# Performance work log

Hardware: AMD Instinct MI355X
Metric: run time of the kernel (lower is better)

The kernel has to match this reference:

```python
import jax, jax.numpy as jnp
import numpy as np

NC = 6          # num_classes
KP = 8          # num_prototype_per_class
NPROTO = NC * KP
PH, PW = 4, 4   # patch grid (num_h, num_w)
MOM = 0.999
EPS = 1e-6


def _layernorm(x, g, b):
    mu = jnp.mean(x, axis=-1, keepdims=True)
    var = jnp.var(x, axis=-1, keepdims=True)
    return (x - mu) / jnp.sqrt(var + EPS) * g + b


def _patch_split(x, nh, nw):
    # (B,C,H,W) -> (B*nh*nw, C, H//nh, W//nw)
    B, C, H, W = x.shape
    ph, pw = H // nh, W // nw
    x = x.reshape(B, C, nh, ph, nw, pw).transpose(0, 2, 4, 1, 3, 5)
    return x.reshape(B * nh * nw, C, ph, pw)


def setup_inputs() -> dict:
    key = jax.random.key(0)
    k1, k2, k3 = jax.random.split(key, 3)
    B, C, Hh, Wh = 8, 128, 128, 128
    Horg, Worg = 512, 512
    return {
        "feats": jax.random.normal(k1, (B, C, Hh, Wh), dtype=jnp.float32),
        "gt": jax.random.randint(k2, (B, Horg, Worg), 0, 7, dtype=jnp.int64),
        "prototype": jax.random.normal(k3, (NPROTO, C), dtype=jnp.float32),
        "ln1_gamma": jnp.ones((C,), jnp.float32),
        "ln1_beta": jnp.zeros((C,), jnp.float32),
        "ln2_gamma": jnp.ones((NPROTO,), jnp.float32),
        "ln2_beta": jnp.zeros((NPROTO,), jnp.float32),
    }


def reference(feats, gt, prototype, ln1_gamma, ln1_beta, ln2_gamma, ln2_beta):
    B, C, Hh, Wh = feats.shape
    Horg, Worg = gt.shape[1], gt.shape[2]

    # --- nearest-neighbor downsample of gt to head resolution (torch 'nearest')
    ih = (jnp.arange(Hh) * Horg) // Hh
    iw = (jnp.arange(Wh) * Worg) // Wh
    label = gt[:, ih[:, None], iw[None, :]]                      # (B,Hh,Wh)
    mask = (label.astype(jnp.int32) != NC).astype(label.dtype)
    one_hot = jax.nn.one_hot(label * mask, NC, dtype=jnp.float32)  # (B,Hh,Wh,NC)
    # torch code does a raw .view(B,-1,Hh,Wh) on the contiguous one-hot; replicate
    pred0 = one_hot.reshape(B, NC, Hh, Wh)

    # --- patch split + spatial gather (softmax-weighted class centers per patch)
    pf = _patch_split(feats, PH, PW)                             # (B*16, C, ph, pw)
    pp = _patch_split(pred0, PH, PW)                             # (B*16, NC, ph, pw)
    bp = pf.shape[0]
    probs = jax.nn.softmax(pp.reshape(bp, NC, -1), axis=2)       # (B*16, NC, HWp)
    fflat = pf.reshape(bp, C, -1)                                # (B*16, C, HWp)
    ctx = jnp.einsum('bkn,bcn->bkc', probs, fflat)               # (B*16, NC, C)

    centers = ctx.reshape(B, PH * PW, NC, C)
    centers = jax.nn.gelu(_layernorm(centers, ln1_gamma, ln1_beta), approximate=False)
    centers = centers.reshape(B, PH * PW * NC, C)                # (B, 96, C)

    # --- nearest prototype assignment (cdist + argmin)
    c2 = jnp.sum(centers * centers, axis=-1)                     # (B,96)
    p2 = jnp.sum(prototype * prototype, axis=-1)                 # (48,)
    d2 = c2[:, :, None] + p2[None, None, :] - 2.0 * jnp.einsum('bmc,kc->bmk', centers, prototype)
    nearest = jnp.argmin(jnp.sqrt(jnp.maximum(d2, 0.0)), axis=-1)  # (B,96)

    # --- sequential, order-dependent momentum EMA scatter update (training path)
    sg = jax.lax.stop_gradient
    idx_flat = nearest.reshape(-1)
    ctr_flat = sg(centers.reshape(-1, C))

    def step(proto, xs):
        i, v = xs
        nv = MOM * proto[i] + (1.0 - MOM) * v
        return proto.at[i].set(nv), None

    proto_val, _ = jax.lax.scan(step, sg(prototype), (idx_flat, ctr_flat))
    # in torch the update writes .data (no grad); downstream grad w.r.t. prototype is identity
    proto_new = prototype + sg(proto_val - prototype)

    # --- prototype-to-pixel cdist similarity map
    nf = feats.reshape(B, C, -1).transpose(0, 2, 1)              # (B,HW,C)
    f2 = jnp.sum(nf * nf, axis=-1)                               # (B,HW)
    pn2 = jnp.sum(proto_new * proto_new, axis=-1)                # (48,)
    d2b = pn2[None, :, None] + f2[:, None, :] - 2.0 * jnp.einsum('kc,bnc->bkn', proto_new, nf)
    distance_l2 = jnp.sqrt(jnp.maximum(d2b, 0.0))                # (B,48,HW)

    p2c = (1.0 / (1.0 + 2.0 * distance_l2)).reshape(B, NPROTO, Hh, Wh)
    p2c = p2c.transpose(0, 2, 3, 1)
    p2c = jax.nn.gelu(_layernorm(p2c, ln2_gamma, ln2_beta), approximate=False)
    p2c_sim_map = p2c.transpose(0, 3, 1, 2)                      # (B,48,Hh,Wh)

    pred = p2c_sim_map.reshape(B, KP, NC, Hh, Wh).max(axis=1)    # (B,NC,Hh,Wh)
    pred = jax.image.resize(pred, (B, NC, Horg, Worg), method='bilinear')

    prototype_expand = jnp.broadcast_to(proto_new, (B, NPROTO, C))
    return pred, prototype_expand, p2c_sim_map, distance_l2, proto_new
```

## Files before the change

kernel.cpp:

```cpp
#include <hip/hip_runtime.h>
#include <hip/hip_bf16.h>
#include <math.h>


#define E_M1 1.71828182845904523536f
#define INV_SQRT2 0.70710678118654752440f

typedef float v2f __attribute__((ext_vector_type(2)));

__device__ __forceinline__ float gelu_exact(float x) {
    return 0.5f * x * (1.f + erff(x * INV_SQRT2));
}
__device__ __forceinline__ v2f splat2(float x) { v2f r; r.x = x; r.y = x; return r; }

__global__ __launch_bounds__(256) void kern0b(const int* __restrict__ gt,
                                              unsigned char* __restrict__ maskb) {
    int idx = blockIdx.x * 256 + threadIdx.x;
    int b = idx >> 14, P = idx & 16383;
    const int* gb = gt + b * 262144;
    unsigned int m = 0;
    #pragma unroll
    for (int c = 0; c < 6; ++c) {
        int pos = c * 16384 + P;
        int hp = pos / 768;
        int rem = pos - hp * 768;
        int wp = rem / 6;
        int kp = rem - wp * 6;
        int g = gb[(4 * hp) * 512 + 4 * wp];
        int lab = (g == 6) ? 0 : g;
        if (lab == kp) m |= (1u << c);
    }
    maskb[idx] = (unsigned char)m;
}

__global__ __launch_bounds__(128) void kernA1(
    const float* __restrict__ feats, const unsigned char* __restrict__ maskb,
    float* __restrict__ part)
{
    const int pidx = blockIdx.x;
    const int patch = pidx >> 2, q = pidx & 3;
    const int b = patch >> 4, pp = patch & 15, ihh = pp >> 2, iww = pp & 3;
    const int c = threadIdx.x;

    const float* fb = feats + (((long long)(b * 128 + c)) * 128 + ihh * 32 + q * 8) * 128 + iww * 32;
    const unsigned char* mb = maskb + b * 16384 + (ihh * 32 + q * 8) * 128 + iww * 32;

    float s0 = 0.f, s1 = 0.f, s2 = 0.f, s3 = 0.f, s4 = 0.f, s5 = 0.f, sall = 0.f;
    for (int r = 0; r < 8; ++r) {
        const float4* row = (const float4*)(fb + r * 128);
        const unsigned int* mr = (const unsigned int*)(mb + r * 128);
        #pragma unroll
        for (int j = 0; j < 8; ++j) {
            float4 v = row[j];
            unsigned int u = mr[j];
            unsigned int b0 = u, b1 = u >> 8, b2 = u >> 16, b3 = u >> 24;
            s0 += ((b0 >> 0) & 1) ? v.x : 0.f;  s1 += ((b0 >> 1) & 1) ? v.x : 0.f;
            s2 += ((b0 >> 2) & 1) ? v.x : 0.f;  s3 += ((b0 >> 3) & 1) ? v.x : 0.f;
            s4 += ((b0 >> 4) & 1) ? v.x : 0.f;  s5 += ((b0 >> 5) & 1) ? v.x : 0.f;
            s0 += ((b1 >> 0) & 1) ? v.y : 0.f;  s1 += ((b1 >> 1) & 1) ? v.y : 0.f;
            s2 += ((b1 >> 2) & 1) ? v.y : 0.f;  s3 += ((b1 >> 3) & 1) ? v.y : 0.f;
            s4 += ((b1 >> 4) & 1) ? v.y : 0.f;  s5 += ((b1 >> 5) & 1) ? v.y : 0.f;
            s0 += ((b2 >> 0) & 1) ? v.z : 0.f;  s1 += ((b2 >> 1) & 1) ? v.z : 0.f;
            s2 += ((b2 >> 2) & 1) ? v.z : 0.f;  s3 += ((b2 >> 3) & 1) ? v.z : 0.f;
            s4 += ((b2 >> 4) & 1) ? v.z : 0.f;  s5 += ((b2 >> 5) & 1) ? v.z : 0.f;
            s0 += ((b3 >> 0) & 1) ? v.w : 0.f;  s1 += ((b3 >> 1) & 1) ? v.w : 0.f;
            s2 += ((b3 >> 2) & 1) ? v.w : 0.f;  s3 += ((b3 >> 3) & 1) ? v.w : 0.f;
            s4 += ((b3 >> 4) & 1) ? v.w : 0.f;  s5 += ((b3 >> 5) & 1) ? v.w : 0.f;
            sall += v.x + v.y + v.z + v.w;
        }
    }
    float* po = part + pidx * 896;
    po[0 * 128 + c] = s0; po[1 * 128 + c] = s1; po[2 * 128 + c] = s2;
    po[3 * 128 + c] = s3; po[4 * 128 + c] = s4; po[5 * 128 + c] = s5;
    po[6 * 128 + c] = sall;
}

__global__ __launch_bounds__(512) void kernA2(
    const float* __restrict__ part, const unsigned char* __restrict__ maskb,
    const float* __restrict__ proto,
    const float* __restrict__ g1, const float* __restrict__ b1,
    float* __restrict__ centersT, int* __restrict__ nearest)
{
    __shared__ float ct[6][128];
    __shared__ int cnt[6];
    __shared__ float pl[48 * 129];

    const int tid = threadIdx.x;
    const int p = blockIdx.x;
    const int b = p >> 4, pp = p & 15, ihh = pp >> 2, iww = pp & 3;

    if (tid < 6) cnt[tid] = 0;
    for (int i = tid; i < 6144; i += 512)
        pl[(i >> 7) * 129 + (i & 127)] = proto[i];
    __syncthreads();

    if (tid < 256) {
        const unsigned char* mb = maskb + b * 16384 + ihh * 32 * 128 + iww * 32;
        int r = tid >> 3, jw = tid & 7;
        unsigned int u = *(const unsigned int*)(mb + r * 128 + jw * 4);
        #pragma unroll
        for (int k = 0; k < 6; ++k) {
            int cc = ((u >> k) & 1) + ((u >> (8 + k)) & 1) +
                     ((u >> (16 + k)) & 1) + ((u >> (24 + k)) & 1);
            #pragma unroll
            for (int m = 1; m < 64; m <<= 1) cc += __shfl_xor(cc, m, 64);
            if ((tid & 63) == 0 && cc) atomicAdd(&cnt[k], cc);
        }
    }
    __syncthreads();

    const float* pb = part + (p * 4) * 896;
    for (int i = tid; i < 768; i += 512) {
        const int c = i & 127, k = i >> 7;
        float Sall = pb[6 * 128 + c] + pb[896 + 6 * 128 + c] +
                     pb[2 * 896 + 6 * 128 + c] + pb[3 * 896 + 6 * 128 + c];
        float Sk = pb[k * 128 + c] + pb[896 + k * 128 + c] +
                   pb[2 * 896 + k * 128 + c] + pb[3 * 896 + k * 128 + c];
        float Z = fmaf((float)cnt[k], E_M1, 1024.f);
        ct[k][c] = (Sall + E_M1 * Sk) / Z;
    }
    __syncthreads();

    const int wv = tid >> 6, lane = tid & 63;
    if (wv < 6) {
        float x0 = ct[wv][lane], x1 = ct[wv][lane + 64];
        float s = x0 + x1;
        #pragma unroll
        for (int m = 1; m < 64; m <<= 1) s += __shfl_xor(s, m, 64);
        float mu = s * (1.f / 128.f);
        float d0 = x0 - mu, d1 = x1 - mu;
        float ss = d0 * d0 + d1 * d1;
        #pragma unroll
        for (int m = 1; m < 64; m <<= 1) ss += __shfl_xor(ss, m, 64);
        float inv = 1.f / sqrtf(ss * (1.f / 128.f) + 1e-6f);
        float y0 = d0 * inv * g1[lane] + b1[lane];
        float y1 = d1 * inv * g1[lane + 64] + b1[lane + 64];
        float z0 = gelu_exact(y0);
        float z1 = gelu_exact(y1);
        const int row = (b * 16 + pp) * 6 + wv;
        centersT[lane * 768 + row] = z0;
        centersT[(lane + 64) * 768 + row] = z1;

        float best = INFINITY; int bi = 0;
        for (int k = 0; k < 48; ++k) {
            float t0 = z0 - pl[k * 129 + lane];
            float t1 = z1 - pl[k * 129 + 64 + lane];
            float sd = fmaf(t0, t0, t1 * t1);
            #pragma unroll
            for (int m = 1; m < 64; m <<= 1) sd += __shfl_xor(sd, m, 64);
            if (sd < best) { best = sd; bi = k; }
        }
        if (lane == 0) nearest[row] = bi;
    }
}

__global__ __launch_bounds__(128) void kernD(
    const float* __restrict__ proto0, const int* __restrict__ nearest,
    const float* __restrict__ centersT,
    float* __restrict__ proto_new, float* __restrict__ pn2,
    float* __restrict__ out_expand, float* __restrict__ out_proto)
{
    __shared__ int nl[768];
    __shared__ float wred[2];
    const int k = blockIdx.x, c = threadIdx.x;
    for (int i = c; i < 768; i += 128) nl[i] = nearest[i];
    __syncthreads();
    float p = proto0[k * 128 + c];
    const float OM = (float)(1.0 - 0.999);
    const float* col = centersT + c * 768;
    #pragma unroll 4
    for (int i = 0; i < 768; i += 4) {
        float4 v = *(const float4*)(col + i);
        if (nl[i + 0] == k) p = 0.999f * p + OM * v.x;
        if (nl[i + 1] == k) p = 0.999f * p + OM * v.y;
        if (nl[i + 2] == k) p = 0.999f * p + OM * v.z;
        if (nl[i + 3] == k) p = 0.999f * p + OM * v.w;
    }
    proto_new[k * 128 + c] = p;
    out_proto[k * 128 + c] = p;
    #pragma unroll
    for (int b = 0; b < 8; ++b) out_expand[(b * 48 + k) * 128 + c] = p;
    float sq = p * p;
    #pragma unroll
    for (int m = 1; m < 64; m <<= 1) sq += __shfl_xor(sq, m, 64);
    if ((c & 63) == 0) wred[c >> 6] = sq;
    __syncthreads();
    if (c == 0) pn2[k] = wred[0] + wred[1];
}

__global__ __launch_bounds__(256) void kernE(
    const float* __restrict__ feats, const float* __restrict__ proto_new,
    const float* __restrict__ pn2g,
    const float* __restrict__ g2, const float* __restrict__ b2,
    float* __restrict__ out_sim, float* __restrict__ out_dist,
    float* __restrict__ pred_small)
{
    __shared__ float smem[16256];
    float* fT   = smem;
    float* prot = smem + 8192;
    float* red  = smem;
    float* dst  = smem + 12672;
    float* p4   = smem + 15808;
    float* F2   = smem + 16064;
    float* muv  = smem + 16128;
    float* invv = smem + 16192;

    const int t = threadIdx.x;
    const int b = blockIdx.y;
    const int nbase = blockIdx.x * 64;

    for (int i4 = t; i4 < 1536; i4 += 256) {
        float4 v = ((const float4*)proto_new)[i4];
        *(float4*)&prot[(i4 >> 5) * 132 + (i4 & 31) * 4] = v;
    }
    #pragma unroll
    for (int it = 0; it < 8; ++it) {
        int idx = it * 256 + t;
        int c = idx >> 4, qd = idx & 15;
        float4 v = *(const float4*)(feats + (((long long)(b * 128 + c)) << 14) + nbase + qd * 4);
        *(float4*)&fT[c * 64 + qd * 4] = v;
    }
    __syncthreads();

    {
        int n = t & 63, cg = t >> 6;
        float s = 0.f;
        for (int c = cg * 32; c < cg * 32 + 32; ++c) { float x = fT[c * 64 + n]; s = fmaf(x, x, s); }
        p4[cg * 64 + n] = s;
    }
    __syncthreads();
    if (t < 64) F2[t] = ((p4[t] + p4[64 + t]) + p4[128 + t]) + p4[192 + t];

    const int w = t >> 6, l = t & 63;
    const int n0 = (l & 7) * 8;
    const int k0 = (l >> 3) * 6;
    const int cbase = w * 32;

    v2f acc[6][4];
    #pragma unroll
    for (int j = 0; j < 6; ++j) {
        #pragma unroll
        for (int h = 0; h < 4; ++h) acc[j][h] = splat2(0.f);
    }

    #pragma unroll 2
    for (int cq = 0; cq < 8; ++cq) {
        const int cb = cbase + cq * 4;
        v2f f[4][4];
        #pragma unroll
        for (int ch = 0; ch < 4; ++ch) {
            float4 a0 = *(const float4*)&fT[(cb + ch) * 64 + n0];
            float4 a1 = *(const float4*)&fT[(cb + ch) * 64 + n0 + 4];
            f[ch][0] = *(v2f*)&a0.x; f[ch][1] = *(v2f*)&a0.z;
            f[ch][2] = *(v2f*)&a1.x; f[ch][3] = *(v2f*)&a1.z;
        }
        #pragma unroll
        for (int j = 0; j < 6; ++j) {
            float4 pv = *(const float4*)&prot[(k0 + j) * 132 + cb];
            v2f px = splat2(pv.x), py = splat2(pv.y), pz = splat2(pv.z), pw = splat2(pv.w);
            #pragma unroll
            for (int h = 0; h < 4; ++h) {
                acc[j][h] = __builtin_elementwise_fma(f[0][h], px,
                            __builtin_elementwise_fma(f[1][h], py,
                            __builtin_elementwise_fma(f[2][h], pz,
                            __builtin_elementwise_fma(f[3][h], pw, acc[j][h]))));
            }
        }
    }
    __syncthreads();

    #pragma unroll
    for (int j = 0; j < 6; ++j) {
        #pragma unroll
        for (int h = 0; h < 4; ++h)
            *(v2f*)&red[w * 3168 + (k0 + j) * 66 + n0 + 2 * h] = acc[j][h];
    }
    __syncthreads();

    for (int cell = t; cell < 768; cell += 256) {
        const int k = cell >> 4, n4 = (cell & 15) * 4;
        v2f lo = splat2(0.f), hi = splat2(0.f);
        #pragma unroll
        for (int ww = 0; ww < 4; ++ww) {
            lo += *(const v2f*)&red[ww * 3168 + k * 66 + n4];
            hi += *(const v2f*)&red[ww * 3168 + k * 66 + n4 + 2];
        }
        float pk = pn2g[k];
        float d0 = sqrtf(fmaxf(F2[n4 + 0] + pk - 2.f * lo.x, 0.f));
        float d1 = sqrtf(fmaxf(F2[n4 + 1] + pk - 2.f * lo.y, 0.f));
        float d2 = sqrtf(fmaxf(F2[n4 + 2] + pk - 2.f * hi.x, 0.f));
        float d3 = sqrtf(fmaxf(F2[n4 + 3] + pk - 2.f * hi.y, 0.f));
        float4 dv; dv.x = d0; dv.y = d1; dv.z = d2; dv.w = d3;
        *(float4*)(out_dist + (((long long)(b * 48 + k)) << 14) + nbase + n4) = dv;
        dst[(n4 + 0) * 49 + k] = 1.f / (1.f + 2.f * d0);
        dst[(n4 + 1) * 49 + k] = 1.f / (1.f + 2.f * d1);
        dst[(n4 + 2) * 49 + k] = 1.f / (1.f + 2.f * d2);
        dst[(n4 + 3) * 49 + k] = 1.f / (1.f + 2.f * d3);
    }
    __syncthreads();

    if (t < 64) {
        const int n = t;
        float s = 0.f;
        for (int k = 0; k < 48; ++k) s += dst[n * 49 + k];
        float mu = s * (1.f / 48.f);
        float s2 = 0.f;
        for (int k = 0; k < 48; ++k) { float d = dst[n * 49 + k] - mu; s2 = fmaf(d, d, s2); }
        muv[n] = mu;
        invv[n] = 1.f / sqrtf(s2 * (1.f / 48.f) + 1e-6f);
    }
    __syncthreads();

    #pragma unroll
    for (int base = 0; base < 384; base += 256) {
        int i = base + t;
        if (i < 384) {
            const int c6 = i >> 6, n = i & 63, ng = nbase + n;
            float mu = muv[n], inv = invv[n];
            float pm = 0.f;
            #pragma unroll
            for (int kp = 0; kp < 8; ++kp) {
                int k = kp * 6 + c6;
                float y = (dst[n * 49 + k] - mu) * inv * g2[k] + b2[k];
                float z = gelu_exact(y);
                out_sim[(((long long)(b * 48 + k)) << 14) + ng] = z;
                pm = (kp == 0) ? z : fmaxf(pm, z);
            }
            pred_small[((b * 6 + c6) << 14) + ng] = pm;
        }
    }
}

__global__ __launch_bounds__(256) void kernF(
    const float* __restrict__ ps, float* __restrict__ pred)
{
    int idx = blockIdx.x * 256 + threadIdx.x;
    int xq = idx & 127;
    int oy = (idx >> 7) & 511;
    int bc = idx >> 16;
    int qy = oy >> 2, ry = oy & 3;
    int y0 = qy + ((ry < 2) ? -1 : 0);
    float fy = (ry == 0) ? 0.625f : (ry == 1) ? 0.875f : (ry == 2) ? 0.125f : 0.375f;
    int y0c = max(y0, 0), y1c = min(y0 + 1, 127);
    const float* base = ps + bc * 16384;
    const float* rA = base + y0c * 128;
    const float* rB = base + y1c * 128;
    int xm = max(xq - 1, 0), xp = min(xq + 1, 127);
    float a0 = rA[xm], a1 = rA[xq], a2 = rA[xp];
    float c0 = rB[xm], c1 = rB[xq], c2 = rB[xp];
    float w0 = 1.f - fy;
    float gm = w0 * a0 + fy * c0;
    float gc = w0 * a1 + fy * c1;
    float gp = w0 * a2 + fy * c2;
    float4 o;
    o.x = 0.375f * gm + 0.625f * gc;
    o.y = 0.125f * gm + 0.875f * gc;
    o.z = 0.875f * gc + 0.125f * gp;
    o.w = 0.625f * gc + 0.375f * gp;
    *(float4*)(pred + ((long long)idx << 2)) = o;
}

extern "C" void kernel_launch(void* const* d_in, const int* in_sizes, int n_in,
                              void* d_out, int out_size, void* d_ws, size_t ws_size,
                              hipStream_t stream)
{
    const float* feats = (const float*)d_in[0];
    const int* gt = (const int*)d_in[1];
    const float* proto = (const float*)d_in[2];
    const float* g1 = (const float*)d_in[3];
    const float* b1 = (const float*)d_in[4];
    const float* g2 = (const float*)d_in[5];
    const float* b2 = (const float*)d_in[6];

    float* out = (float*)d_out;
    float* pred       = out;
    float* out_expand = out + 12582912;
    float* out_sim    = out + 12632064;
    float* out_dist   = out + 18923520;
    float* out_proto  = out + 25214976;

    float* ws = (float*)d_ws;
    float* centersT   = ws + 98304;
    float* proto_new  = ws + 196608;
    float* pn2        = ws + 202752;
    int*   nearest    = (int*)(ws + 202816);
    float* part       = ws + 203584;
    float* pred_small = ws + 203584;
    unsigned char* maskb = (unsigned char*)(ws + 990016);

    kern0b<<<512, 256, 0, stream>>>(gt, maskb);
    kernA1<<<512, 128, 0, stream>>>(feats, maskb, part);
    kernA2<<<128, 512, 0, stream>>>(part, maskb, proto, g1, b1, centersT, nearest);
    kernD <<<48, 128, 0, stream>>>(proto, nearest, centersT, proto_new, pn2,
                                   out_expand, out_proto);
    kernE <<<dim3(256, 8), 256, 0, stream>>>(feats, proto_new, pn2, g2, b2,
                                             out_sim, out_dist, pred_small);
    kernF <<<12288, 256, 0, stream>>>(pred_small, pred);
}
```

Baseline: 270.1 us.

## Double threads per block in feature-reduction and similarity kernels

kernA1 now uses 256 threads and splits each patch quarter's rows between two halves, combining the partial sums through shared memory. kernE moves to 512 threads: each wave covers half the pixel columns in the dot-product tile, and the LayerNorm statistics are computed in parallel across 256 threads using a single-pass sum and sum of squares. The goal is more parallelism and latency hiding in these memory-bound kernels. In exchange it adds a barrier and shared-memory traffic, and the single-pass variance formula is less numerically robust.

```diff
diff --git a/kernel.cpp b/kernel.cpp
--- a/kernel.cpp
+++ b/kernel.cpp
@@ -33,20 +33,22 @@
     maskb[idx] = (unsigned char)m;
 }
 
-__global__ __launch_bounds__(128) void kernA1(
+__global__ __launch_bounds__(256) void kernA1(
     const float* __restrict__ feats, const unsigned char* __restrict__ maskb,
     float* __restrict__ part)
 {
+    __shared__ float accs[7][128];
     const int pidx = blockIdx.x;
     const int patch = pidx >> 2, q = pidx & 3;
     const int b = patch >> 4, pp = patch & 15, ihh = pp >> 2, iww = pp & 3;
-    const int c = threadIdx.x;
-
-    const float* fb = feats + (((long long)(b * 128 + c)) * 128 + ihh * 32 + q * 8) * 128 + iww * 32;
-    const unsigned char* mb = maskb + b * 16384 + (ihh * 32 + q * 8) * 128 + iww * 32;
+    const int c = threadIdx.x & 127, sub = threadIdx.x >> 7;
+
+    const int row0 = ihh * 32 + q * 8 + sub * 4;
+    const float* fb = feats + (((long long)(b * 128 + c)) * 128 + row0) * 128 + iww * 32;
+    const unsigned char* mb = maskb + b * 16384 + row0 * 128 + iww * 32;
 
     float s0 = 0.f, s1 = 0.f, s2 = 0.f, s3 = 0.f, s4 = 0.f, s5 = 0.f, sall = 0.f;
-    for (int r = 0; r < 8; ++r) {
+    for (int r = 0; r < 4; ++r) {
         const float4* row = (const float4*)(fb + r * 128);
         const unsigned int* mr = (const unsigned int*)(mb + r * 128);
         #pragma unroll
@@ -69,10 +71,21 @@
             sall += v.x + v.y + v.z + v.w;
         }
     }
-    float* po = part + pidx * 896;
-    po[0 * 128 + c] = s0; po[1 * 128 + c] = s1; po[2 * 128 + c] = s2;
-    po[3 * 128 + c] = s3; po[4 * 128 + c] = s4; po[5 * 128 + c] = s5;
-    po[6 * 128 + c] = sall;
+    if (sub == 1) {
+        accs[0][c] = s0; accs[1][c] = s1; accs[2][c] = s2; accs[3][c] = s3;
+        accs[4][c] = s4; accs[5][c] = s5; accs[6][c] = sall;
+    }
+    __syncthreads();
+    if (sub == 0) {
+        float* po = part + pidx * 896;
+        po[0 * 128 + c] = s0 + accs[0][c];
+        po[1 * 128 + c] = s1 + accs[1][c];
+        po[2 * 128 + c] = s2 + accs[2][c];
+        po[3 * 128 + c] = s3 + accs[3][c];
+        po[4 * 128 + c] = s4 + accs[4][c];
+        po[5 * 128 + c] = s5 + accs[5][c];
+        po[6 * 128 + c] = sall + accs[6][c];
+    }
 }
 
 __global__ __launch_bounds__(512) void kernA2(
@@ -188,34 +201,36 @@
     if (c == 0) pn2[k] = wred[0] + wred[1];
 }
 
-__global__ __launch_bounds__(256) void kernE(
+__global__ __launch_bounds__(512) void kernE(
     const float* __restrict__ feats, const float* __restrict__ proto_new,
     const float* __restrict__ pn2g,
     const float* __restrict__ g2, const float* __restrict__ b2,
     float* __restrict__ out_sim, float* __restrict__ out_dist,
     float* __restrict__ pred_small)
 {
-    __shared__ float smem[16256];
+    __shared__ float smem[16000];
     float* fT   = smem;
     float* prot = smem + 8192;
+    float* p4   = smem + 14528;
     float* red  = smem;
     float* dst  = smem + 12672;
-    float* p4   = smem + 15808;
-    float* F2   = smem + 16064;
-    float* muv  = smem + 16128;
-    float* invv = smem + 16192;
+    float* lnA  = smem;
+    float* lnB  = smem + 256;
+    float* F2   = smem + 15808;
+    float* muv  = smem + 15872;
+    float* invv = smem + 15936;
 
     const int t = threadIdx.x;
     const int b = blockIdx.y;
     const int nbase = blockIdx.x * 64;
 
-    for (int i4 = t; i4 < 1536; i4 += 256) {
+    for (int i4 = t; i4 < 1536; i4 += 512) {
         float4 v = ((const float4*)proto_new)[i4];
         *(float4*)&prot[(i4 >> 5) * 132 + (i4 & 31) * 4] = v;
     }
     #pragma unroll
-    for (int it = 0; it < 8; ++it) {
-        int idx = it * 256 + t;
+    for (int it = 0; it < 4; ++it) {
+        int idx = it * 512 + t;
         int c = idx >> 4, qd = idx & 15;
         float4 v = *(const float4*)(feats + (((long long)(b * 128 + c)) << 14) + nbase + qd * 4);
         *(float4*)&fT[c * 64 + qd * 4] = v;
@@ -225,41 +240,42 @@
     {
         int n = t & 63, cg = t >> 6;
         float s = 0.f;
-        for (int c = cg * 32; c < cg * 32 + 32; ++c) { float x = fT[c * 64 + n]; s = fmaf(x, x, s); }
+        for (int c = cg * 16; c < cg * 16 + 16; ++c) { float x = fT[c * 64 + n]; s = fmaf(x, x, s); }
         p4[cg * 64 + n] = s;
     }
     __syncthreads();
-    if (t < 64) F2[t] = ((p4[t] + p4[64 + t]) + p4[128 + t]) + p4[192 + t];
+    if (t < 64) {
+        float s = 0.f;
+        #pragma unroll
+        for (int g = 0; g < 8; ++g) s += p4[g * 64 + t];
+        F2[t] = s;
+    }
 
     const int w = t >> 6, l = t & 63;
-    const int n0 = (l & 7) * 8;
+    const int cw = w & 3, nh = w >> 2;
+    const int n0 = nh * 32 + (l & 7) * 4;
     const int k0 = (l >> 3) * 6;
-    const int cbase = w * 32;
-
-    v2f acc[6][4];
-    #pragma unroll
-    for (int j = 0; j < 6; ++j) {
-        #pragma unroll
-        for (int h = 0; h < 4; ++h) acc[j][h] = splat2(0.f);
-    }
-
-    #pragma unroll 2
+    const int cbase = cw * 32;
+
+    v2f acc[6][2];
+    #pragma unroll
+    for (int j = 0; j < 6; ++j) { acc[j][0] = splat2(0.f); acc[j][1] = splat2(0.f); }
+
+    #pragma unroll
     for (int cq = 0; cq < 8; ++cq) {
         const int cb = cbase + cq * 4;
-        v2f f[4][4];
+        v2f f[4][2];
         #pragma unroll
         for (int ch = 0; ch < 4; ++ch) {
             float4 a0 = *(const float4*)&fT[(cb + ch) * 64 + n0];
-            float4 a1 = *(const float4*)&fT[(cb + ch) * 64 + n0 + 4];
             f[ch][0] = *(v2f*)&a0.x; f[ch][1] = *(v2f*)&a0.z;
-            f[ch][2] = *(v2f*)&a1.x; f[ch][3] = *(v2f*)&a1.z;
         }
         #pragma unroll
         for (int j = 0; j < 6; ++j) {
             float4 pv = *(const float4*)&prot[(k0 + j) * 132 + cb];
             v2f px = splat2(pv.x), py = splat2(pv.y), pz = splat2(pv.z), pw = splat2(pv.w);
             #pragma unroll
-            for (int h = 0; h < 4; ++h) {
+            for (int h = 0; h < 2; ++h) {
                 acc[j][h] = __builtin_elementwise_fma(f[0][h], px,
                             __builtin_elementwise_fma(f[1][h], py,
                             __builtin_elementwise_fma(f[2][h], pz,
@@ -271,13 +287,12 @@
 
     #pragma unroll
     for (int j = 0; j < 6; ++j) {
-        #pragma unroll
-        for (int h = 0; h < 4; ++h)
-            *(v2f*)&red[w * 3168 + (k0 + j) * 66 + n0 + 2 * h] = acc[j][h];
-    }
-    __syncthreads();
-
-    for (int cell = t; cell < 768; cell += 256) {
+        *(v2f*)&red[cw * 3168 + (k0 + j) * 66 + n0]     = acc[j][0];
+        *(v2f*)&red[cw * 3168 + (k0 + j) * 66 + n0 + 2] = acc[j][1];
+    }
+    __syncthreads();
+
+    for (int cell = t; cell < 768; cell += 512) {
         const int k = cell >> 4, n4 = (cell & 15) * 4;
         v2f lo = splat2(0.f), hi = splat2(0.f);
         #pragma unroll
@@ -299,35 +314,40 @@
     }
     __syncthreads();
 
+    if (t < 256) {
+        const int n = t & 63, q = t >> 6;
+        float s1 = 0.f, s2 = 0.f;
+        for (int k = q * 12; k < q * 12 + 12; ++k) {
+            float x = dst[n * 49 + k];
+            s1 += x; s2 = fmaf(x, x, s2);
+        }
+        lnA[q * 64 + n] = s1;
+        lnB[q * 64 + n] = s2;
+    }
+    __syncthreads();
     if (t < 64) {
-        const int n = t;
-        float s = 0.f;
-        for (int k = 0; k < 48; ++k) s += dst[n * 49 + k];
-        float mu = s * (1.f / 48.f);
-        float s2 = 0.f;
-        for (int k = 0; k < 48; ++k) { float d = dst[n * 49 + k] - mu; s2 = fmaf(d, d, s2); }
-        muv[n] = mu;
-        invv[n] = 1.f / sqrtf(s2 * (1.f / 48.f) + 1e-6f);
-    }
-    __syncthreads();
-
-    #pragma unroll
-    for (int base = 0; base < 384; base += 256) {
-        int i = base + t;
-        if (i < 384) {
-            const int c6 = i >> 6, n = i & 63, ng = nbase + n;
-            float mu = muv[n], inv = invv[n];
-            float pm = 0.f;
-            #pragma unroll
-            for (int kp = 0; kp < 8; ++kp) {
-                int k = kp * 6 + c6;
-                float y = (dst[n * 49 + k] - mu) * inv * g2[k] + b2[k];
-                float z = gelu_exact(y);
-                out_sim[(((long long)(b * 48 + k)) << 14) + ng] = z;
-                pm = (kp == 0) ? z : fmaxf(pm, z);
-            }
-            pred_small[((b * 6 + c6) << 14) + ng] = pm;
-        }
+        float s1 = ((lnA[t] + lnA[64 + t]) + lnA[128 + t]) + lnA[192 + t];
+        float s2 = ((lnB[t] + lnB[64 + t]) + lnB[128 + t]) + lnB[192 + t];
+        float mu = s1 * (1.f / 48.f);
+        float var = fmaxf(s2 * (1.f / 48.f) - mu * mu, 0.f);
+        muv[t] = mu;
+        invv[t] = 1.f / sqrtf(var + 1e-6f);
+    }
+    __syncthreads();
+
+    if (t < 384) {
+        const int c6 = t >> 6, n = t & 63, ng = nbase + n;
+        float mu = muv[n], inv = invv[n];
+        float pm = 0.f;
+        #pragma unroll
+        for (int kp = 0; kp < 8; ++kp) {
+            int k = kp * 6 + c6;
+            float y = (dst[n * 49 + k] - mu) * inv * g2[k] + b2[k];
+            float z = gelu_exact(y);
+            out_sim[(((long long)(b * 48 + k)) << 14) + ng] = z;
+            pm = (kp == 0) ? z : fmaxf(pm, z);
+        }
+        pred_small[((b * 6 + c6) << 14) + ng] = pm;
     }
 }
 
@@ -389,11 +409,11 @@
     unsigned char* maskb = (unsigned char*)(ws + 990016);
 
     kern0b<<<512, 256, 0, stream>>>(gt, maskb);
-    kernA1<<<512, 128, 0, stream>>>(feats, maskb, part);
+    kernA1<<<512, 256, 0, stream>>>(feats, maskb, part);
     kernA2<<<128, 512, 0, stream>>>(part, maskb, proto, g1, b1, centersT, nearest);
     kernD <<<48, 128, 0, stream>>>(proto, nearest, centersT, proto_new, pn2,
                                    out_expand, out_proto);
-    kernE <<<dim3(256, 8), 256, 0, stream>>>(feats, proto_new, pn2, g2, b2,
+    kernE <<<dim3(256, 8), 512, 0, stream>>>(feats, proto_new, pn2, g2, b2,
                                              out_sim, out_dist, pred_small);
     kernF <<<12288, 256, 0, stream>>>(pred_small, pred);
 }
```

Result: faster. 259.8 us (-3.8%).
